# Kernel tuning notes

Hardware: AMD Instinct MI355X
Metric: run time of the kernel (lower is better)

The kernel has to match this reference:

```python
import jax, jax.numpy as jnp
import numpy as np

B, T, H, P = 256, 512, 512, 128


def _lstm_cell(x, h, c, Wih, Whh, bih, bhh):
    # torch.nn.LSTMCell math: gates = x@Wih^T + bih + h@Whh^T + bhh, chunks i,f,g,o
    gates = x @ Wih.T + h @ Whh.T + (bih + bhh)
    i, f, g, o = jnp.split(gates, 4, axis=-1)
    c2 = jax.nn.sigmoid(f) * c + jax.nn.sigmoid(i) * jnp.tanh(g)
    h2 = jax.nn.sigmoid(o) * jnp.tanh(c2)
    return h2, c2


def setup_inputs() -> dict:
    key = jax.random.key(0)
    ks = jax.random.split(key, 12)
    s = 0.1
    return {
        "x": jax.random.normal(ks[0], (B, T), dtype=jnp.float32),
        "enc_Wih": jax.random.normal(ks[1], (4 * H, 1), dtype=jnp.float32) * s,
        "enc_Whh": jax.random.normal(ks[2], (4 * H, H), dtype=jnp.float32) * s,
        "enc_bih": jax.random.normal(ks[3], (4 * H,), dtype=jnp.float32) * s,
        "enc_bhh": jax.random.normal(ks[4], (4 * H,), dtype=jnp.float32) * s,
        "dec_Wih": jax.random.normal(ks[5], (4 * H, H), dtype=jnp.float32) * s,
        "dec_Whh": jax.random.normal(ks[6], (4 * H, H), dtype=jnp.float32) * s,
        "dec_bih": jax.random.normal(ks[7], (4 * H,), dtype=jnp.float32) * s,
        "dec_bhh": jax.random.normal(ks[8], (4 * H,), dtype=jnp.float32) * s,
        "dense_W": jax.random.normal(ks[9], (1, H), dtype=jnp.float32) * s,
        "dense_b": jax.random.normal(ks[10], (1,), dtype=jnp.float32) * s,
        "predict_length": P,
    }


def reference(x, enc_Wih, enc_Whh, enc_bih, enc_bhh,
              dec_Wih, dec_Whh, dec_bih, dec_bhh,
              dense_W, dense_b, predict_length):
    batch = x.shape[0]
    x3 = x[:, :, None]  # [B, T, 1]
    h0 = jnp.zeros((batch, H), dtype=x.dtype)
    c0 = jnp.zeros((batch, H), dtype=x.dtype)

    # Encoder: scan over time
    def enc_step(carry, xt):
        h, c = carry
        h, c = _lstm_cell(xt, h, c, enc_Wih, enc_Whh, enc_bih, enc_bhh)
        return (h, c), None

    (h, c), _ = jax.lax.scan(enc_step, (h0, c0), jnp.transpose(x3, (1, 0, 2)))

    # Decoder loop (faithful to original: decoder state updated but unused for x;
    # encoder is re-run from the frozen (h, c) each step)
    def dec_step(carry, _):
        xc, nh, nc = carry
        nh2, nc2 = _lstm_cell(xc, nh, nc, dec_Wih, dec_Whh, dec_bih, dec_bhh)
        y = xc @ dense_W.T + dense_b            # [B, 1]
        x_next, _ = _lstm_cell(y, h, c, enc_Wih, enc_Whh, enc_bih, enc_bhh)
        return (x_next, nh2, nc2), y

    _, ys = jax.lax.scan(dec_step, (h, h, c), None, length=predict_length)
    # ys: [P, B, 1] -> [B, P]
    return jnp.transpose(ys[:, :, 0], (1, 0))
```

## Files before the change

### kernel.cpp

```cpp
#include <hip/hip_runtime.h>

#define B_ 256
#define T_ 512
#define H_ 512
#define P_ 128
#define G4 2048

typedef __attribute__((ext_vector_type(8))) _Float16 h8_t;
typedef __attribute__((ext_vector_type(4))) float floatx4;

__device__ __forceinline__ float sigm(float x){ return 1.0f / (1.0f + __expf(-x)); }
__device__ __forceinline__ float tanh_(float x){ return 2.0f / (1.0f + __expf(-2.0f*x)) - 1.0f; }
__device__ __forceinline__ unsigned short f2h(float f){
  union { _Float16 h; unsigned short u; } c; c.h = (_Float16)f; return c.u;
}
__device__ __forceinline__ float wredsum(float v){
  #pragma unroll
  for (int off = 32; off; off >>= 1) v += __shfl_xor(v, off, 64);
  return v;
}

__global__ __launch_bounds__(256) void pack_w(const float* __restrict__ Whh,
                                              unsigned short* __restrict__ Wp){
  int p8   = blockIdx.x * 256 + threadIdx.x;
  int lane = p8 & 63;
  int kt   = (p8 >> 6) & 15;
  int ct   = (p8 >> 10) & 1;
  int w    = (p8 >> 11) & 3;
  int cg   = (p8 >> 13) & 15;
  int q    = (lane & 15) >> 2, dhc = lane & 3;
  int col  = q*512 + cg*32 + w*8 + ct*4 + dhc;
  int k0   = kt*32 + (lane >> 4)*8;
  const float* s = Whh + (size_t)col * H_ + k0;
  unsigned short v[8];
  #pragma unroll
  for (int e = 0; e < 8; e++) v[e] = f2h(s[e]);
  *(uint4*)(Wp + (size_t)p8 * 8) = *(const uint4*)v;
}

__global__ __launch_bounds__(256) void enc_persist(
    const unsigned short* __restrict__ Wp,
    const float* __restrict__ x,
    const float* __restrict__ Wih,
    const float* __restrict__ bih,
    const float* __restrict__ bhh,
    unsigned long long* __restrict__ X,
    float* __restrict__ hfp,
    float* __restrict__ cfin,
    float* __restrict__ G,
    int zf)
{
  __shared__ float x_lds[16][512];
  __shared__ uint4 A_lds4[1024];
  __shared__ float Sg[4][16][33];
  __shared__ char pad_[30000];

  char* A_lds = (char*)A_lds4;
  const int bid = blockIdx.x;
  const int bg = bid >> 4, cg = bid & 15;
  const int tid = threadIdx.x;
  const int lane = tid & 63, wv = tid >> 6;

  if (zf){ pad_[tid] = (char)Wih[tid]; if (!tid) A_lds[0] = pad_[128]; }

  h8_t wreg[2][16];
  {
    const unsigned short* wb = Wp + (size_t)((cg*4 + wv)*2) * 8192;
    #pragma unroll
    for (int ct = 0; ct < 2; ct++)
      #pragma unroll
      for (int kt = 0; kt < 16; kt++)
        wreg[ct][kt] = *(const h8_t*)(wb + (ct*16 + kt)*512 + lane*8);
  }
  #pragma unroll
  for (int i = 0; i < 8; i++){
    int idx = tid + i*256;
    int r = idx >> 7, c4 = (idx & 127)*4;
    *(float4*)&x_lds[r][c4] = *(const float4*)&x[(size_t)(bg*16 + r)*T_ + c4];
  }
  const int erow = tid >> 4;
  const int hp   = tid & 15;
  const int hc0  = cg*32 + hp*2;
  float wih0[4], wih1[4], bs0[4], bs1[4];
  #pragma unroll
  for (int q = 0; q < 4; q++){
    wih0[q] = Wih[q*512 + hc0];     wih1[q] = Wih[q*512 + hc0 + 1];
    bs0[q]  = bih[q*512 + hc0]     + bhh[q*512 + hc0];
    bs1[q]  = bih[q*512 + hc0 + 1] + bhh[q*512 + hc0 + 1];
  }
  float cr0 = 0.f, cr1 = 0.f;

  const size_t Xrow = (size_t)(bg*16 + erow)*256 + hp;
  int lws[16];
  #pragma unroll
  for (int j = 0; j < 16; j++){
    int cp = hp + j*16;
    lws[j] = erow*1024 + ((cp*4) ^ ((erow & 7) << 4));
  }
  const int arow = lane & 15, ahalf = lane >> 4;
  const int rxor = (arow & 7) << 4;
  const size_t pidx = (size_t)(bg*16 + erow)*256 + cg*16 + hp;

  for (int t = 0; t <= T_; t++){
    unsigned long long* Xb = X + (size_t)((t+1)&1) * 65536;
    const unsigned wtag = (unsigned)t;
    unsigned pend = 0xFFFFu;
    do {
      unsigned long long tmp[16];
      #pragma unroll
      for (int j = 0; j < 16; j++)
        if (pend & (1u << j))
          tmp[j] = __hip_atomic_load(Xb + Xrow + j*16, __ATOMIC_RELAXED,
                                     __HIP_MEMORY_SCOPE_AGENT);
      unsigned np = 0u;
      #pragma unroll
      for (int j = 0; j < 16; j++){
        if (pend & (1u << j)){
          if ((unsigned)(tmp[j] >> 32) == wtag)
            *(unsigned*)(A_lds + lws[j]) = (unsigned)tmp[j];
          else
            np |= 1u << j;
        }
      }
      pend = np;
      if (pend) __builtin_amdgcn_s_sleep(1);
    } while (pend);
    __syncthreads();

    floatx4 acc0 = {0,0,0,0}, acc1 = {0,0,0,0};
    h8_t a[16];
    #pragma unroll
    for (int kt = 0; kt < 16; kt++)
      a[kt] = *(const h8_t*)(A_lds + arow*1024 + ((kt*64 + ahalf*16) ^ rxor));
    #pragma unroll
    for (int kt = 0; kt < 16; kt++){
      acc0 = __builtin_amdgcn_mfma_f32_16x16x32_f16(a[kt], wreg[0][kt], acc0, 0,0,0);
      acc1 = __builtin_amdgcn_mfma_f32_16x16x32_f16(a[kt], wreg[1][kt], acc1, 0,0,0);
    }
    #pragma unroll
    for (int r = 0; r < 4; r++){
      int srow = ahalf*4 + r;
      int q = (lane & 15) >> 2, dhc = lane & 3;
      Sg[q][srow][wv*8 + dhc]     = acc0[r];
      Sg[q][srow][wv*8 + 4 + dhc] = acc1[r];
    }
    __syncthreads();

    if (t == T_){
      int b = bg*16 + erow;
      #pragma unroll
      for (int q = 0; q < 4; q++){
        G[(size_t)b*G4 + q*512 + hc0]     = Sg[q][erow][hp*2]     + bs0[q];
        G[(size_t)b*G4 + q*512 + hc0 + 1] = Sg[q][erow][hp*2 + 1] + bs1[q];
      }
      break;
    }

    const float xb = x_lds[erow][t];
    float pi0 = Sg[0][erow][hp*2] + xb*wih0[0] + bs0[0];
    float pf0 = Sg[1][erow][hp*2] + xb*wih0[1] + bs0[1];
    float pg0 = Sg[2][erow][hp*2] + xb*wih0[2] + bs0[2];
    float po0 = Sg[3][erow][hp*2] + xb*wih0[3] + bs0[3];
    float c20 = sigm(pf0)*cr0 + sigm(pi0)*tanh_(pg0);
    float h0  = sigm(po0)*tanh_(c20);  cr0 = c20;

    float pi1 = Sg[0][erow][hp*2+1] + xb*wih1[0] + bs1[0];
    float pf1 = Sg[1][erow][hp*2+1] + xb*wih1[1] + bs1[1];
    float pg1 = Sg[2][erow][hp*2+1] + xb*wih1[2] + bs1[2];
    float po1 = Sg[3][erow][hp*2+1] + xb*wih1[3] + bs1[3];
    float c21 = sigm(pf1)*cr1 + sigm(pi1)*tanh_(c21*0.f + pg1*0.f + pg1);
    c21 = sigm(pf1)*cr1 + sigm(pi1)*tanh_(pg1);
    float h1  = sigm(po1)*tanh_(c21);  cr1 = c21;

    if (t == T_-1){
      int b = bg*16 + erow;
      hfp[(size_t)b*512 + hc0]     = h0;  hfp[(size_t)b*512 + hc0 + 1] = h1;
      cfin[(size_t)b*512 + hc0]    = c20; cfin[(size_t)b*512 + hc0 + 1] = c21;
    }
    unsigned pay = (unsigned)f2h(h0) | ((unsigned)f2h(h1) << 16);
    unsigned long long wo = ((unsigned long long)(t + 1) << 32) | pay;
    (void)__hip_atomic_exchange(X + (size_t)(t & 1)*65536 + pidx, wo,
                                __ATOMIC_RELAXED, __HIP_MEMORY_SCOPE_AGENT);
  }
}

__global__ __launch_bounds__(256) void decoder(
    const float* __restrict__ G, const float* __restrict__ c,
    const float* __restrict__ hfp, const float* __restrict__ Wih,
    const float* __restrict__ dW, const float* __restrict__ db,
    float* __restrict__ out)
{
  const int row  = blockIdx.x * 4 + (threadIdx.x >> 6);
  const int lane = threadIdx.x & 63;
  float Gr[4][8], wr[4][8], cc[8], wd[8];
  float p = 0.f;
  #pragma unroll
  for (int k = 0; k < 8; k++){
    int j = lane + k*64;
    cc[k] = c[(size_t)row*H_ + j];
    wd[k] = dW[j];
    #pragma unroll
    for (int q = 0; q < 4; q++){
      Gr[q][k] = G[(size_t)row*G4 + q*512 + j];
      wr[q][k] = Wih[q*512 + j];
    }
    p += hfp[(size_t)row*H_ + j] * wd[k];
  }
  const float bias = db[0];
  float y = wredsum(p) + bias;
  for (int tt = 0; tt < P_; tt++){
    if (lane == 0) out[(size_t)row*P_ + tt] = y;
    if (tt == P_-1) break;
    float pp = 0.f;
    #pragma unroll
    for (int k = 0; k < 8; k++){
      float i_ = sigm (y*wr[0][k] + Gr[0][k]);
      float f_ = sigm (y*wr[1][k] + Gr[1][k]);
      float g_ = tanh_(y*wr[2][k] + Gr[2][k]);
      float o_ = sigm (y*wr[3][k] + Gr[3][k]);
      float c2 = f_*cc[k] + i_*g_;
      pp += o_*tanh_(c2)*wd[k];
    }
    y = wredsum(pp) + bias;
  }
}

extern "C" void kernel_launch(void* const* d_in, const int* in_sizes, int n_in,
                              void* d_out, int out_size, void* d_ws, size_t ws_size,
                              hipStream_t stream)
{
  const float* x    = (const float*)d_in[0];
  const float* Wih  = (const float*)d_in[1];
  const float* Whh  = (const float*)d_in[2];
  const float* bih  = (const float*)d_in[3];
  const float* bhh  = (const float*)d_in[4];
  const float* dW   = (const float*)d_in[9];
  const float* db   = (const float*)d_in[10];
  float* out = (float*)d_out;

  unsigned short* Wp    = (unsigned short*)d_ws;
  unsigned long long* X = (unsigned long long*)(Wp + 1048576);
  float* hfp  = (float*)(X + 131072);
  float* cfin = hfp + 131072;
  float* G    = cfin + 131072;

  hipMemsetAsync(X + 65536, 0, 65536 * sizeof(unsigned long long), stream);
  pack_w<<<512, 256, 0, stream>>>(Whh, Wp);
  enc_persist<<<256, 256, 0, stream>>>(Wp, x, Wih, bih, bhh, X,
                                       hfp, cfin, G, 0);
  decoder<<<64, 256, 0, stream>>>(G, cfin, hfp, Wih, dW, db, out);
}
```

Before: 1.936 ms.

## Split each block's batch rows into two interleaved half-tiles to overlap recurrence phases

Each persistent encoder block now handles two groups of 8 batch rows (one from each half of the batch) and processes them as alternating phases per timestep, with the MFMA run on a half-filled 16-row A tile whose upper rows are zeroed. The intent is for one group's cross-block wait to overlap with the other group's compute, hiding the inter-block synchronisation latency of the recurrent chain. Each thread now owns a single hidden column and pairs with its neighbour via shuffle to publish packed fp16 values. The cost is double the MFMA and barrier count per timestep, with half the MMA rows wasted, and more complex flag polling.

```diff
diff --git a/kernel.cpp b/kernel.cpp
--- a/kernel.cpp
+++ b/kernel.cpp
@@ -53,13 +53,14 @@
   __shared__ float x_lds[16][512];
   __shared__ uint4 A_lds4[1024];
   __shared__ float Sg[4][16][33];
-  __shared__ char pad_[30000];
+  __shared__ char pad_[26000];
 
   char* A_lds = (char*)A_lds4;
   const int bid = blockIdx.x;
-  const int bg = bid >> 4, cg = bid & 15;
+  const int g = bid >> 4, cg = bid & 15;
   const int tid = threadIdx.x;
   const int lane = tid & 63, wv = tid >> 6;
+  const int rA = g*8, rB = 128 + g*8;
 
   if (zf){ pad_[tid] = (char)Wih[tid]; if (!tid) A_lds[0] = pad_[128]; }
 
@@ -76,45 +77,53 @@
   for (int i = 0; i < 8; i++){
     int idx = tid + i*256;
     int r = idx >> 7, c4 = (idx & 127)*4;
-    *(float4*)&x_lds[r][c4] = *(const float4*)&x[(size_t)(bg*16 + r)*T_ + c4];
-  }
-  const int erow = tid >> 4;
-  const int hp   = tid & 15;
-  const int hc0  = cg*32 + hp*2;
-  float wih0[4], wih1[4], bs0[4], bs1[4];
+    int grow = (r < 8) ? (rA + r) : (rB + r - 8);
+    *(float4*)&x_lds[r][c4] = *(const float4*)&x[(size_t)grow*T_ + c4];
+  }
+  {
+    uint4 z = {0,0,0,0};
+    *(uint4*)(A_lds + 8192 + tid*32)      = z;
+    *(uint4*)(A_lds + 8192 + tid*32 + 16) = z;
+  }
+
+  const int erow = tid >> 5, hc = tid & 31;
+  const int hcg  = cg*32 + hc;
+  float wih[4], bs[4];
   #pragma unroll
   for (int q = 0; q < 4; q++){
-    wih0[q] = Wih[q*512 + hc0];     wih1[q] = Wih[q*512 + hc0 + 1];
-    bs0[q]  = bih[q*512 + hc0]     + bhh[q*512 + hc0];
-    bs1[q]  = bih[q*512 + hc0 + 1] + bhh[q*512 + hc0 + 1];
-  }
-  float cr0 = 0.f, cr1 = 0.f;
-
-  const size_t Xrow = (size_t)(bg*16 + erow)*256 + hp;
-  int lws[16];
-  #pragma unroll
-  for (int j = 0; j < 16; j++){
-    int cp = hp + j*16;
+    wih[q] = Wih[q*512 + hcg];
+    bs[q]  = bih[q*512 + hcg] + bhh[q*512 + hcg];
+  }
+  float crA = 0.f, crB = 0.f;
+
+  int lws[8];
+  #pragma unroll
+  for (int j = 0; j < 8; j++){
+    int cp = hc + j*32;
     lws[j] = erow*1024 + ((cp*4) ^ ((erow & 7) << 4));
   }
+  const size_t XrowA = (size_t)(rA + erow)*256 + hc;
+  const size_t XrowB = (size_t)(rB + erow)*256 + hc;
+  const size_t pA = (size_t)(rA + erow)*256 + cg*16 + (hc >> 1);
+  const size_t pB = (size_t)(rB + erow)*256 + cg*16 + (hc >> 1);
   const int arow = lane & 15, ahalf = lane >> 4;
   const int rxor = (arow & 7) << 4;
-  const size_t pidx = (size_t)(bg*16 + erow)*256 + cg*16 + hp;
-
-  for (int t = 0; t <= T_; t++){
+
+  auto phase = [&](int t, int xrow0, size_t Xrow, size_t pidx, int grow,
+                   float& cr) {
     unsigned long long* Xb = X + (size_t)((t+1)&1) * 65536;
     const unsigned wtag = (unsigned)t;
-    unsigned pend = 0xFFFFu;
+    unsigned pend = 0xFFu;
     do {
-      unsigned long long tmp[16];
-      #pragma unroll
-      for (int j = 0; j < 16; j++)
+      unsigned long long tmp[8];
+      #pragma unroll
+      for (int j = 0; j < 8; j++)
         if (pend & (1u << j))
-          tmp[j] = __hip_atomic_load(Xb + Xrow + j*16, __ATOMIC_RELAXED,
+          tmp[j] = __hip_atomic_load(Xb + Xrow + j*32, __ATOMIC_RELAXED,
                                      __HIP_MEMORY_SCOPE_AGENT);
       unsigned np = 0u;
       #pragma unroll
-      for (int j = 0; j < 16; j++){
+      for (int j = 0; j < 8; j++){
         if (pend & (1u << j)){
           if ((unsigned)(tmp[j] >> 32) == wtag)
             *(unsigned*)(A_lds + lws[j]) = (unsigned)tmp[j];
@@ -147,40 +156,36 @@
     __syncthreads();
 
     if (t == T_){
-      int b = bg*16 + erow;
-      #pragma unroll
-      for (int q = 0; q < 4; q++){
-        G[(size_t)b*G4 + q*512 + hc0]     = Sg[q][erow][hp*2]     + bs0[q];
-        G[(size_t)b*G4 + q*512 + hc0 + 1] = Sg[q][erow][hp*2 + 1] + bs1[q];
-      }
-      break;
-    }
-
-    const float xb = x_lds[erow][t];
-    float pi0 = Sg[0][erow][hp*2] + xb*wih0[0] + bs0[0];
-    float pf0 = Sg[1][erow][hp*2] + xb*wih0[1] + bs0[1];
-    float pg0 = Sg[2][erow][hp*2] + xb*wih0[2] + bs0[2];
-    float po0 = Sg[3][erow][hp*2] + xb*wih0[3] + bs0[3];
-    float c20 = sigm(pf0)*cr0 + sigm(pi0)*tanh_(pg0);
-    float h0  = sigm(po0)*tanh_(c20);  cr0 = c20;
-
-    float pi1 = Sg[0][erow][hp*2+1] + xb*wih1[0] + bs1[0];
-    float pf1 = Sg[1][erow][hp*2+1] + xb*wih1[1] + bs1[1];
-    float pg1 = Sg[2][erow][hp*2+1] + xb*wih1[2] + bs1[2];
-    float po1 = Sg[3][erow][hp*2+1] + xb*wih1[3] + bs1[3];
-    float c21 = sigm(pf1)*cr1 + sigm(pi1)*tanh_(c21*0.f + pg1*0.f + pg1);
-    c21 = sigm(pf1)*cr1 + sigm(pi1)*tanh_(pg1);
-    float h1  = sigm(po1)*tanh_(c21);  cr1 = c21;
-
+      #pragma unroll
+      for (int q = 0; q < 4; q++)
+        G[(size_t)grow*G4 + q*512 + hcg] = Sg[q][erow][hc] + bs[q];
+      return;
+    }
+
+    const float xb = x_lds[xrow0 + erow][t];
+    float pi = Sg[0][erow][hc] + xb*wih[0] + bs[0];
+    float pf = Sg[1][erow][hc] + xb*wih[1] + bs[1];
+    float pg = Sg[2][erow][hc] + xb*wih[2] + bs[2];
+    float po = Sg[3][erow][hc] + xb*wih[3] + bs[3];
+    float c2 = sigm(pf)*cr + sigm(pi)*tanh_(pg);
+    float h2 = sigm(po)*tanh_(c2);
+    cr = c2;
     if (t == T_-1){
-      int b = bg*16 + erow;
-      hfp[(size_t)b*512 + hc0]     = h0;  hfp[(size_t)b*512 + hc0 + 1] = h1;
-      cfin[(size_t)b*512 + hc0]    = c20; cfin[(size_t)b*512 + hc0 + 1] = c21;
-    }
-    unsigned pay = (unsigned)f2h(h0) | ((unsigned)f2h(h1) << 16);
-    unsigned long long wo = ((unsigned long long)(t + 1) << 32) | pay;
-    (void)__hip_atomic_exchange(X + (size_t)(t & 1)*65536 + pidx, wo,
-                                __ATOMIC_RELAXED, __HIP_MEMORY_SCOPE_AGENT);
+      hfp [(size_t)grow*512 + hcg] = h2;
+      cfin[(size_t)grow*512 + hcg] = c2;
+    }
+    float hо = __shfl_xor(h2, 1);
+    if (!(lane & 1)){
+      unsigned pay = (unsigned)f2h(h2) | ((unsigned)f2h(hо) << 16);
+      unsigned long long wo = ((unsigned long long)(t + 1) << 32) | pay;
+      (void)__hip_atomic_exchange(X + (size_t)(t & 1)*65536 + pidx, wo,
+                                  __ATOMIC_RELAXED, __HIP_MEMORY_SCOPE_AGENT);
+    }
+  };
+
+  for (int t = 0; t <= T_; t++){
+    phase(t, 0, XrowA, pA, rA + erow, crA);
+    phase(t, 8, XrowB, pB, rB + erow, crB);
   }
 }
 
@@ -244,7 +249,7 @@
   float* cfin = hfp + 131072;
   float* G    = cfin + 131072;
 
-  hipMemsetAsync(X + 65536, 0, 65536 * sizeof(unsigned long long), stream);
+  hipMemsetAsync(X, 0, 131072 * sizeof(unsigned long long), stream);
   pack_w<<<512, 256, 0, stream>>>(Whh, Wp);
   enc_persist<<<256, 256, 0, stream>>>(Wp, x, Wih, bih, bhh, X,
                                        hfp, cfin, G, 0);
```

New measurement: 2.018 ms. 1.04x slower.

## Assign encoder roles by XCC and use volatile polling without sleep

Applied to the files above, without the earlier changes.

Each workgroup reads its XCC id from a hardware register and takes a role from a per-XCC atomic counter. This places the 16 column-group blocks that share a batch group on the same XCC, so their h exchanges can stay in that XCC's L2 instead of crossing dies. The flag spin loop uses volatile loads and stores instead of agent-scope atomics and no longer sleeps between polls, aiming to cut handoff latency per timestep. The mapping assumes exactly 32 blocks land on each of 8 XCCs, and volatile accesses may not be coherent across XCCs, so the scheme risks stale reads or hangs if placement differs.

```diff
diff --git a/kernel.cpp b/kernel.cpp
--- a/kernel.cpp
+++ b/kernel.cpp
@@ -48,20 +48,30 @@
     float* __restrict__ hfp,
     float* __restrict__ cfin,
     float* __restrict__ G,
+    unsigned* __restrict__ cnt,
     int zf)
 {
   __shared__ float x_lds[16][512];
   __shared__ uint4 A_lds4[1024];
   __shared__ float Sg[4][16][33];
   __shared__ char pad_[30000];
+  __shared__ int role_s;
 
   char* A_lds = (char*)A_lds4;
-  const int bid = blockIdx.x;
-  const int bg = bid >> 4, cg = bid & 15;
   const int tid = threadIdx.x;
   const int lane = tid & 63, wv = tid >> 6;
 
   if (zf){ pad_[tid] = (char)Wih[tid]; if (!tid) A_lds[0] = pad_[128]; }
+
+  if (tid == 0){
+    unsigned xcc = __builtin_amdgcn_s_getreg(14356) & 7u;
+    unsigned s = __hip_atomic_fetch_add(&cnt[xcc], 1u, __ATOMIC_RELAXED,
+                                        __HIP_MEMORY_SCOPE_AGENT);
+    role_s = (int)(xcc*32u + s);
+  }
+  __syncthreads();
+  const int role = role_s;
+  const int g = role >> 4, cg = role & 15;
 
   h8_t wreg[2][16];
   {
@@ -76,7 +86,7 @@
   for (int i = 0; i < 8; i++){
     int idx = tid + i*256;
     int r = idx >> 7, c4 = (idx & 127)*4;
-    *(float4*)&x_lds[r][c4] = *(const float4*)&x[(size_t)(bg*16 + r)*T_ + c4];
+    *(float4*)&x_lds[r][c4] = *(const float4*)&x[(size_t)(g*16 + r)*T_ + c4];
   }
   const int erow = tid >> 4;
   const int hp   = tid & 15;
@@ -90,7 +100,7 @@
   }
   float cr0 = 0.f, cr1 = 0.f;
 
-  const size_t Xrow = (size_t)(bg*16 + erow)*256 + hp;
+  const size_t Xrow = (size_t)(g*16 + erow)*256 + hp;
   int lws[16];
   #pragma unroll
   for (int j = 0; j < 16; j++){
@@ -99,19 +109,18 @@
   }
   const int arow = lane & 15, ahalf = lane >> 4;
   const int rxor = (arow & 7) << 4;
-  const size_t pidx = (size_t)(bg*16 + erow)*256 + cg*16 + hp;
+  const size_t pidx = (size_t)(g*16 + erow)*256 + cg*16 + hp;
 
   for (int t = 0; t <= T_; t++){
-    unsigned long long* Xb = X + (size_t)((t+1)&1) * 65536;
+    const volatile unsigned long long* Xv =
+        (const volatile unsigned long long*)(X + (size_t)((t+1)&1) * 65536);
     const unsigned wtag = (unsigned)t;
     unsigned pend = 0xFFFFu;
     do {
       unsigned long long tmp[16];
       #pragma unroll
       for (int j = 0; j < 16; j++)
-        if (pend & (1u << j))
-          tmp[j] = __hip_atomic_load(Xb + Xrow + j*16, __ATOMIC_RELAXED,
-                                     __HIP_MEMORY_SCOPE_AGENT);
+        if (pend & (1u << j)) tmp[j] = Xv[Xrow + j*16];
       unsigned np = 0u;
       #pragma unroll
       for (int j = 0; j < 16; j++){
@@ -123,7 +132,6 @@
         }
       }
       pend = np;
-      if (pend) __builtin_amdgcn_s_sleep(1);
     } while (pend);
     __syncthreads();
 
@@ -147,7 +155,7 @@
     __syncthreads();
 
     if (t == T_){
-      int b = bg*16 + erow;
+      int b = g*16 + erow;
       #pragma unroll
       for (int q = 0; q < 4; q++){
         G[(size_t)b*G4 + q*512 + hc0]     = Sg[q][erow][hp*2]     + bs0[q];
@@ -168,19 +176,17 @@
     float pf1 = Sg[1][erow][hp*2+1] + xb*wih1[1] + bs1[1];
     float pg1 = Sg[2][erow][hp*2+1] + xb*wih1[2] + bs1[2];
     float po1 = Sg[3][erow][hp*2+1] + xb*wih1[3] + bs1[3];
-    float c21 = sigm(pf1)*cr1 + sigm(pi1)*tanh_(c21*0.f + pg1*0.f + pg1);
-    c21 = sigm(pf1)*cr1 + sigm(pi1)*tanh_(pg1);
+    float c21 = sigm(pf1)*cr1 + sigm(pi1)*tanh_(pg1);
     float h1  = sigm(po1)*tanh_(c21);  cr1 = c21;
 
     if (t == T_-1){
-      int b = bg*16 + erow;
+      int b = g*16 + erow;
       hfp[(size_t)b*512 + hc0]     = h0;  hfp[(size_t)b*512 + hc0 + 1] = h1;
       cfin[(size_t)b*512 + hc0]    = c20; cfin[(size_t)b*512 + hc0 + 1] = c21;
     }
     unsigned pay = (unsigned)f2h(h0) | ((unsigned)f2h(h1) << 16);
     unsigned long long wo = ((unsigned long long)(t + 1) << 32) | pay;
-    (void)__hip_atomic_exchange(X + (size_t)(t & 1)*65536 + pidx, wo,
-                                __ATOMIC_RELAXED, __HIP_MEMORY_SCOPE_AGENT);
+    *(volatile unsigned long long*)(X + (size_t)(t & 1)*65536 + pidx) = wo;
   }
 }
 
@@ -243,10 +249,12 @@
   float* hfp  = (float*)(X + 131072);
   float* cfin = hfp + 131072;
   float* G    = cfin + 131072;
-
-  hipMemsetAsync(X + 65536, 0, 65536 * sizeof(unsigned long long), stream);
+  unsigned* cnt = (unsigned*)(G + 524288);
+
+  hipMemsetAsync(X, 0, 131072 * sizeof(unsigned long long), stream);
+  hipMemsetAsync(cnt, 0, 64, stream);
   pack_w<<<512, 256, 0, stream>>>(Whh, Wp);
   enc_persist<<<256, 256, 0, stream>>>(Wp, x, Wih, bih, bhh, X,
-                                       hfp, cfin, G, 0);
+                                       hfp, cfin, G, cnt, 0);
   decoder<<<64, 256, 0, stream>>>(G, cfin, hfp, Wih, dW, db, out);
 }
```

New measurement: 3.736 ms. 92.9% more time.
